# Optimization experiments

Hardware: AMD Instinct MI355X
Metric: run time of the kernel (lower is better)

## Reference

```python
import jax, jax.numpy as jnp
import numpy as np

B, H, W, C = 8, 256, 256, 180
HEADS, HEAD_DIM = 6, 30
WIN = (16, 16)
SPARSITY = 4


def setup_inputs() -> dict:
    key = jax.random.key(0)
    ks = jax.random.split(key, 6)
    bg = 1.0 / np.sqrt(3 * HEAD_DIM)          # ExpertGather init bound (1/sqrt(head_dim_out)) approx
    bs = 1.0 / np.sqrt(C * HEADS)             # ExpertScatter init bound
    return {
        "x": jax.random.normal(ks[0], (B, H, W, C), jnp.float32),
        "Wr": jax.random.normal(ks[1], (HEADS, C), jnp.float32) / np.sqrt(C),      # router Linear(dim, heads, bias=False)
        "Wqkv": jax.random.uniform(ks[2], (HEADS, C, 3 * HEAD_DIM), jnp.float32, -bg, bg),
        "Wo": jax.random.uniform(ks[3], (HEADS, HEAD_DIM, C), jnp.float32, -bs, bs),
        "Wp": jax.random.normal(ks[4], (C, C), jnp.float32) / np.sqrt(C),          # proj Linear(dim, dim)
        "bp": jnp.zeros((C,), jnp.float32),
    }


def reference(x, Wr, Wqkv, Wo, Wp, bp):
    wh, ww = WIN
    L = wh * ww  # tokens per window = 256
    # ---- window_partition: (B,H,W,C) -> (Bw, L, C)
    xw = x.reshape(B, H // wh, wh, W // ww, ww, C).transpose(0, 1, 3, 2, 4, 5).reshape(-1, L, C)
    Bw = xw.shape[0]
    # ---- router: sigmoid(Linear) -> (Bw, L, heads)
    logits = jax.nn.sigmoid(jnp.einsum('blc,ec->ble', xw, Wr))
    k = min(max(L // SPARSITY, 2), L)  # static: 64
    # ---- top-k including first token (get_topk_includefirst)
    tail = logits[:, 1:, :].transpose(0, 2, 1)          # (Bw, heads, L-1)
    tv, ti = jax.lax.top_k(tail, k - 1)                 # top k-1 over tokens 1..L-1
    ti = ti + 1
    fv = logits[:, 0, :][:, :, None]                    # (Bw, heads, 1)
    fi = jnp.zeros((Bw, HEADS, 1), jnp.int32)
    vals = jnp.concatenate([fv, tv], axis=2)            # (Bw, heads, k) sigmoid gates
    idx = jnp.concatenate([fi, ti], axis=2)             # (Bw, heads, k) token indices
    idx_flat = idx.reshape(Bw, HEADS * k)
    # ---- ExpertGather: per-head gather then per-head linear -> QKV
    Xg = jnp.take_along_axis(xw, idx_flat[:, :, None], axis=1).reshape(Bw, HEADS, k, C)
    qkv = jnp.einsum('beki,eij->bekj', Xg, Wqkv)        # (Bw, heads, k, 3*head_dim)
    Q, K, V = jnp.split(qkv, 3, axis=-1)
    # ---- scaled dot product attention over the k routed tokens per head
    scores = jnp.einsum('bekd,bejd->bekj', Q, K) / np.sqrt(HEAD_DIM).astype(np.float32)
    attn = jnp.einsum('bekj,bejd->bekd', jax.nn.softmax(scores, axis=-1), V)
    attn = attn * vals[..., None]                       # sigmoid gating
    # ---- ExpertScatter: per-head linear then scatter-add combine
    pre = jnp.einsum('bekj,eji->beki', attn, Wo)        # (Bw, heads, k, C)
    scattered = jnp.zeros((Bw, L, C), x.dtype).at[
        jnp.arange(Bw)[:, None], idx_flat
    ].add(pre.reshape(Bw, HEADS * k, C))
    # ---- window_reverse: (Bw, L, C) -> (B, H, W, C)
    y = scattered.reshape(B, H // wh, W // ww, wh, ww, C).transpose(0, 1, 3, 2, 4, 5).reshape(B, H, W, C)
    # ---- output projection (dropout prob = 0)
    return jnp.einsum('bhwc,oc->bhwo', y, Wp) + bp
```

## Files before the change

### kernel.cpp

```cpp
#include <hip/hip_runtime.h>
#include <math.h>

#define NB 8
#define NH 256
#define NW 256
#define NC 180
#define NE 6
#define HD 30
#define NL 256
#define NK 64
#define NWIN 2048

typedef __attribute__((ext_vector_type(8))) short bf16x8;
typedef __attribute__((ext_vector_type(4))) float f32x4;

union FU { bf16x8 f; unsigned u[4]; unsigned short s[8]; };

static __device__ __forceinline__ unsigned short f2bf(float x) {
    unsigned u = __float_as_uint(x);
    unsigned r = (u + 0x7FFFu + ((u >> 16) & 1u)) >> 16;
    return (unsigned short)r;
}
static __device__ __forceinline__ unsigned pk2(float a, float b) {
    return (unsigned)f2bf(a) | ((unsigned)f2bf(b) << 16);
}
static __device__ __forceinline__ bf16x8 ld8(const unsigned short* p) {
    FU t;
    *(uint2*)&t.u[0] = *(const uint2*)p;
    *(uint2*)&t.u[2] = *(const uint2*)(p + 16);
    return t.f;
}
static __device__ __forceinline__ bf16x8 ld8q(const unsigned short* p) {
    FU t;
    t.u[0] = *(const unsigned*)p;
    t.u[1] = *(const unsigned*)(p + 2);
    t.u[2] = *(const unsigned*)(p + 16);
    t.u[3] = *(const unsigned*)(p + 18);
    return t.f;
}
static __device__ __forceinline__ bf16x8 pack8(float4 a, float4 b) {
    FU t;
    t.u[0] = pk2(a.x, a.y); t.u[1] = pk2(a.z, a.w);
    t.u[2] = pk2(b.x, b.y); t.u[3] = pk2(b.z, b.w);
    return t.f;
}

__global__ __launch_bounds__(256) void k_prep(
    const float* __restrict__ Wqkv, const float* __restrict__ Wo,
    const float* __restrict__ Wp,
    unsigned short* __restrict__ Wqkv_t, unsigned short* __restrict__ Wcomb_t)
{
    int i = blockIdx.x * 256 + threadIdx.x;
    if (i < NE * 96 * 192) {
        int h = i / (96 * 192), rm = i % (96 * 192), np = rm / 192, k = rm % 192;
        int sec = np >> 5, r = np & 31;
        float v = (r < 30 && k < NC) ? Wqkv[((long)h * NC + k) * 90 + sec * 30 + r] : 0.f;
        Wqkv_t[i] = f2bf(v);
    }
    if (i < NE * 192 * 32) {
        int h = i / (192 * 32), rm = i % (192 * 32), o = rm / 32, d = rm & 31;
        float acc = 0.f;
        if (o < NC && d < HD) {
            const float* wo = Wo + ((long)h * HD + d) * NC;
            const float* wp = Wp + (long)o * NC;
            for (int c = 0; c < NC; ++c) acc += wo[c] * wp[c];
        }
        Wcomb_t[i] = f2bf(acc);
    }
}

__global__ __launch_bounds__(256) void k_router_topk(
    const float* __restrict__ x, const float* __restrict__ Wr,
    int* __restrict__ idx_g, float* __restrict__ vals_g)
{
    __shared__ float wr_s[NE * NC];
    __shared__ __align__(16) float xs[32 * 181];
    __shared__ float lg[NE * NL];

    const int w   = blockIdx.x;
    const int tid = threadIdx.x;
    const int b = w >> 8, hb = (w >> 4) & 15, wb = w & 15;
    const long win_base = (((long)b * NH + hb * 16) * NW + wb * 16) * NC;

    for (int f = tid; f < NE * NC; f += 256) wr_s[f] = Wr[f];
    __syncthreads();

    for (int tile = 0; tile < 8; ++tile) {
        for (int f = tid; f < 32 * NC; f += 256) {
            int tl = f / NC, ch = f % NC;
            int tok = tile * 32 + tl;
            int r = tok >> 4, cl = tok & 15;
            xs[tl * 181 + ch] = x[win_base + ((long)r * NW + cl) * NC + ch];
        }
        __syncthreads();
        if (tid < 192) {
            int tl = tid & 31, e = tid >> 5;
            float acc = 0.f;
            for (int c = 0; c < NC; ++c) acc += xs[tl * 181 + c] * wr_s[e * NC + c];
            lg[e * NL + tile * 32 + tl] = 1.0f / (1.0f + expf(-acc));
        }
        __syncthreads();
    }

    unsigned long long* keys = (unsigned long long*)xs;
    #pragma unroll
    for (int e = 0; e < NE; ++e) {
        unsigned kb = __float_as_uint(lg[e * NL + tid]);
        unsigned long long comp =
            ((unsigned long long)kb << 32) | (unsigned)(0xFFFFFFFFu - tid);
        if (tid == 0) comp = 0ull;
        keys[e * NL + tid] = comp;
    }
    __syncthreads();

    for (int k = 2; k <= 256; k <<= 1) {
        for (int j = k >> 1; j > 0; j >>= 1) {
            const int i = tid, ixj = i ^ j;
            if (ixj > i) {
                const bool up = ((i & k) == 0);
                #pragma unroll
                for (int e = 0; e < NE; ++e) {
                    unsigned long long a  = keys[e * NL + i];
                    unsigned long long bv = keys[e * NL + ixj];
                    bool sw = up ? (a < bv) : (a > bv);
                    if (sw) { keys[e * NL + i] = bv; keys[e * NL + ixj] = a; }
                }
            }
            __syncthreads();
        }
    }

    if (tid < NK - 1) {
        #pragma unroll
        for (int e = 0; e < NE; ++e) {
            unsigned long long kk = keys[e * NL + tid];
            int t = (int)(0xFFFFFFFFu - (unsigned)kk);
            idx_g[(w * NE + e) * NK + 1 + tid]  = t;
            vals_g[(w * NE + e) * NK + 1 + tid] = __uint_as_float((unsigned)(kk >> 32));
        }
    }
    if (tid == 0) {
        #pragma unroll
        for (int e = 0; e < NE; ++e) {
            idx_g[(w * NE + e) * NK]  = 0;
            vals_g[(w * NE + e) * NK] = lg[e * NL];
        }
    }
}

__global__ __launch_bounds__(256, 3) void k_attn(
    const float* __restrict__ x,
    const unsigned short* __restrict__ Wqkv_t,
    const int* __restrict__ idx_g, const float* __restrict__ vals_g,
    unsigned short* __restrict__ at_g)
{
    __shared__ char sm[34816];
    const int tid = threadIdx.x;
    const int wv = tid >> 6;
    const int ln = tid & 63;
    const int lr = ln & 15;
    const int lg = ln >> 4;

    const int id = blockIdx.x * 4 + wv;
    const int w = id / 6;
    const int h = id % 6;
    const int b = w >> 8, hb = (w >> 4) & 15, wb = w & 15;
    const long win_base = (((long)b * NH + hb * 16) * NW + wb * 16) * NC;

    unsigned short* q_s = (unsigned short*)(sm + wv * 8704);
    unsigned short* k_s = q_s + 2176;

    int tokr[4];
    #pragma unroll
    for (int t = 0; t < 4; ++t)
        tokr[t] = idx_g[((long)w * NE + h) * NK + 16 * t + lr];

    f32x4 acc[6][4];
    #pragma unroll
    for (int nt = 0; nt < 6; ++nt)
        #pragma unroll
        for (int mt = 0; mt < 4; ++mt) acc[nt][mt] = (f32x4){0.f, 0.f, 0.f, 0.f};

    const unsigned short* bb = Wqkv_t + ((long)h * 96 + lr) * 192 + 4 * lg;
    #pragma unroll
    for (int kt = 0; kt < 6; ++kt) {
        bf16x8 Amt[4];
        #pragma unroll
        for (int mt = 0; mt < 4; ++mt) {
            const float* xr = x + win_base +
                ((long)(tokr[mt] >> 4) * NW + (tokr[mt] & 15)) * NC;
            if (kt < 5) {
                float4 a  = *(const float4*)(xr + 4 * lg + 32 * kt);
                float4 b2 = *(const float4*)(xr + 4 * lg + 32 * kt + 16);
                Amt[mt] = pack8(a, b2);
            } else {
                float4 a  = *(const float4*)(xr + 4 * lg + 160);
                float4 b2 = make_float4(0.f, 0.f, 0.f, 0.f);
                if (lg == 0) b2 = *(const float4*)(xr + 176);
                Amt[mt] = pack8(a, b2);
            }
        }
        #pragma unroll
        for (int nt = 0; nt < 6; ++nt) {
            bf16x8 B = ld8(bb + nt * (16 * 192) + kt * 32);
            #pragma unroll
            for (int mt = 0; mt < 4; ++mt)
                acc[nt][mt] = __builtin_amdgcn_mfma_f32_16x16x32_bf16(Amt[mt], B, acc[nt][mt], 0, 0, 0);
        }
    }

    #pragma unroll
    for (int nt = 0; nt < 4; ++nt) {
        unsigned short* dst = (nt < 2 ? q_s : k_s) + 16 * (nt & 1) + lr;
        #pragma unroll
        for (int mt = 0; mt < 4; ++mt) {
            int row = 16 * mt + 4 * lg;
            dst[(row + 0) * 34] = f2bf(acc[nt][mt][0]);
            dst[(row + 1) * 34] = f2bf(acc[nt][mt][1]);
            dst[(row + 2) * 34] = f2bf(acc[nt][mt][2]);
            dst[(row + 3) * 34] = f2bf(acc[nt][mt][3]);
        }
    }
    unsigned V32[4][2][2];
    #pragma unroll
    for (int j = 0; j < 2; ++j)
        #pragma unroll
        for (int mt = 0; mt < 4; ++mt) {
            V32[mt][j][0] = pk2(acc[4 + j][mt][0], acc[4 + j][mt][1]);
            V32[mt][j][1] = pk2(acc[4 + j][mt][2], acc[4 + j][mt][3]);
        }

    __syncthreads();

    f32x4 s[4][4];
    {
        bf16x8 Bq[4];
        #pragma unroll
        for (int nt = 0; nt < 4; ++nt)
            Bq[nt] = ld8q(q_s + (16 * nt + lr) * 34 + 4 * lg);
        #pragma unroll
        for (int amt = 0; amt < 4; ++amt) {
            bf16x8 Ak = ld8q(k_s + (16 * amt + lr) * 34 + 4 * lg);
            #pragma unroll
            for (int nt = 0; nt < 4; ++nt)
                s[amt][nt] = __builtin_amdgcn_mfma_f32_16x16x32_bf16(
                    Ak, Bq[nt], (f32x4){0.f, 0.f, 0.f, 0.f}, 0, 0, 0);
        }
    }

    float gsc[4];
    #pragma unroll
    for (int nt = 0; nt < 4; ++nt) {
        float mx = -1e30f;
        #pragma unroll
        for (int amt = 0; amt < 4; ++amt)
            #pragma unroll
            for (int r = 0; r < 4; ++r) mx = fmaxf(mx, s[amt][nt][r]);
        mx = fmaxf(mx, __shfl_xor(mx, 16));
        mx = fmaxf(mx, __shfl_xor(mx, 32));
        float sum = 0.f;
        #pragma unroll
        for (int amt = 0; amt < 4; ++amt)
            #pragma unroll
            for (int r = 0; r < 4; ++r) {
                float p = __expf((s[amt][nt][r] - mx) * 0.18257418583505536f);
                s[amt][nt][r] = p;
                sum += p;
            }
        sum += __shfl_xor(sum, 16);
        sum += __shfl_xor(sum, 32);
        gsc[nt] = vals_g[((long)w * NE + h) * NK + 16 * nt + lr] / sum;
    }

    bf16x8 Av[2][2];
    #pragma unroll
    for (int amt = 0; amt < 2; ++amt)
        #pragma unroll
        for (int kt = 0; kt < 2; ++kt) {
            FU t;
            t.u[0] = V32[2 * kt][amt][0];
            t.u[1] = V32[2 * kt][amt][1];
            t.u[2] = V32[2 * kt + 1][amt][0];
            t.u[3] = V32[2 * kt + 1][amt][1];
            Av[amt][kt] = t.f;
        }
    #pragma unroll
    for (int nt = 0; nt < 4; ++nt) {
        bf16x8 Pb[2];
        float g = gsc[nt];
        #pragma unroll
        for (int kt = 0; kt < 2; ++kt) {
            FU t;
            t.u[0] = pk2(s[2 * kt][nt][0] * g, s[2 * kt][nt][1] * g);
            t.u[1] = pk2(s[2 * kt][nt][2] * g, s[2 * kt][nt][3] * g);
            t.u[2] = pk2(s[2 * kt + 1][nt][0] * g, s[2 * kt + 1][nt][1] * g);
            t.u[3] = pk2(s[2 * kt + 1][nt][2] * g, s[2 * kt + 1][nt][3] * g);
            Pb[kt] = t.f;
        }
        f32x4 a0 = (f32x4){0.f, 0.f, 0.f, 0.f};
        a0 = __builtin_amdgcn_mfma_f32_16x16x32_bf16(Av[0][0], Pb[0], a0, 0, 0, 0);
        a0 = __builtin_amdgcn_mfma_f32_16x16x32_bf16(Av[0][1], Pb[1], a0, 0, 0, 0);
        f32x4 a1 = (f32x4){0.f, 0.f, 0.f, 0.f};
        a1 = __builtin_amdgcn_mfma_f32_16x16x32_bf16(Av[1][0], Pb[0], a1, 0, 0, 0);
        a1 = __builtin_amdgcn_mfma_f32_16x16x32_bf16(Av[1][1], Pb[1], a1, 0, 0, 0);
        unsigned short* row = at_g + (((long)h * NWIN + w) * 64 + 16 * nt + lr) * 32;
        *(uint2*)(row + 4 * lg)      = make_uint2(pk2(a0[0], a0[1]), pk2(a0[2], a0[3]));
        *(uint2*)(row + 16 + 4 * lg) = make_uint2(pk2(a1[0], a1[1]), pk2(a1[2], a1[3]));
    }
}

__global__ __launch_bounds__(384, 2) void k_scatter(
    const unsigned short* __restrict__ at_g,
    const unsigned short* __restrict__ Wcomb_t,
    const float* __restrict__ bp,
    const int* __restrict__ idx_g,
    float* __restrict__ out)
{
    __shared__ float outf[256 * 49];
    __shared__ unsigned char idx_s[NE * NK];

    const int w = blockIdx.x;
    const int tid = threadIdx.x;
    const int b = w >> 8, hb = (w >> 4) & 15, wb = w & 15;

    const int wv = tid >> 6;
    const int ln = tid & 63;
    const int lr = ln & 15;
    const int lg = ln >> 4;

    idx_s[tid] = (unsigned char)idx_g[(long)w * NE * NK + tid];

    const int wcol = wv % 3;
    const int nth  = wv / 3;

    bf16x8 Bt[NE][2];
    #pragma unroll
    for (int h = 0; h < NE; ++h)
        #pragma unroll
        for (int t = 0; t < 2; ++t) {
            const int nt = 2 * nth + t;
            Bt[h][t] = ld8(at_g + (((long)h * NWIN + w) * 64 + 16 * nt + lr) * 32 + 4 * lg);
        }
    __syncthreads();

    int tokk[NE][2];
    #pragma unroll
    for (int h = 0; h < NE; ++h)
        #pragma unroll
        for (int t = 0; t < 2; ++t)
            tokk[h][t] = idx_s[h * NK + 16 * (2 * nth + t) + lr];

    #pragma unroll
    for (int p = 0; p < 4; ++p) {
        for (int f = tid; f < 256 * 49; f += 384) outf[f] = 0.f;
        __syncthreads();

        #pragma unroll
        for (int h = 0; h < NE; ++h) {
            bf16x8 Aw = ld8(Wcomb_t + ((long)h * 192 + p * 48 + 16 * wcol + lr) * 32 + 4 * lg);
            #pragma unroll
            for (int t = 0; t < 2; ++t) {
                f32x4 acc = __builtin_amdgcn_mfma_f32_16x16x32_bf16(
                    Aw, Bt[h][t], (f32x4){0.f, 0.f, 0.f, 0.f}, 0, 0, 0);
                float* dst = outf + tokk[h][t] * 49 + 16 * wcol + 4 * lg;
                dst[0] += acc[0];
                dst[1] += acc[1];
                dst[2] += acc[2];
                dst[3] += acc[3];
            }
            __syncthreads();
        }

        const int nf4 = (p == 3) ? 9 : 12;
        for (int f = tid; f < 256 * nf4; f += 384) {
            int t = f / nf4, j = f % nf4;
            int c = 48 * p + 4 * j;
            float4 o;
            o.x = outf[t * 49 + 4 * j]     + bp[c];
            o.y = outf[t * 49 + 4 * j + 1] + bp[c + 1];
            o.z = outf[t * 49 + 4 * j + 2] + bp[c + 2];
            o.w = outf[t * 49 + 4 * j + 3] + bp[c + 3];
            long obase = (((long)b * NH + hb * 16 + (t >> 4)) * NW + wb * 16 + (t & 15)) * NC + c;
            *(float4*)(out + obase) = o;
        }
        __syncthreads();
    }
}

extern "C" void kernel_launch(void* const* d_in, const int* in_sizes, int n_in,
                              void* d_out, int out_size, void* d_ws, size_t ws_size,
                              hipStream_t stream) {
    const float* x    = (const float*)d_in[0];
    const float* Wr   = (const float*)d_in[1];
    const float* Wqkv = (const float*)d_in[2];
    const float* Wo   = (const float*)d_in[3];
    const float* Wp   = (const float*)d_in[4];
    const float* bp   = (const float*)d_in[5];
    float* out = (float*)d_out;

    char* ws = (char*)d_ws;
    unsigned short* Wqkv_t  = (unsigned short*)ws;
    unsigned short* Wcomb_t = (unsigned short*)(ws + 221184);
    int*   idx_g  = (int*)(ws + 294912);
    float* vals_g = (float*)(ws + 294912 + (size_t)NWIN * NE * NK * 4);
    unsigned short* at_g = (unsigned short*)(ws + 294912 + 2 * (size_t)NWIN * NE * NK * 4);

    k_prep<<<432, 256, 0, stream>>>(Wqkv, Wo, Wp, Wqkv_t, Wcomb_t);
    k_router_topk<<<NWIN, 256, 0, stream>>>(x, Wr, idx_g, vals_g);
    k_attn<<<3072, 256, 0, stream>>>(x, Wqkv_t, idx_g, vals_g, at_g);
    k_scatter<<<NWIN, 384, 0, stream>>>(at_g, Wcomb_t, bp, idx_g, out);
}
```

Before: 598.5 us.

## Pre-swizzle bf16 weight and attention layouts for 16-byte vector loads; remap block order

Reorders the packed Wqkv, combined Wo·Wp and attention-output buffers so that each lane's eight MFMA operand elements are contiguous. Two 8-byte loads become one 16-byte load in the attention and scatter kernels, and the attention store becomes a single 16-byte write. It also permutes the attention kernel's block index, likely to spread work across XCDs or improve cache locality. The layout has to stay consistent between the producer and consumer kernels, and the gains are limited to operand-load instruction count.

Result: faster. 569.4 us (-4.9%).

```diff
diff --git a/kernel.cpp b/kernel.cpp
--- a/kernel.cpp
+++ b/kernel.cpp
@@ -30,6 +30,11 @@
     *(uint2*)&t.u[2] = *(const uint2*)(p + 16);
     return t.f;
 }
+static __device__ __forceinline__ bf16x8 ld16(const unsigned short* p) {
+    FU t;
+    *(uint4*)&t.u[0] = *(const uint4*)p;
+    return t.f;
+}
 static __device__ __forceinline__ bf16x8 ld8q(const unsigned short* p) {
     FU t;
     t.u[0] = *(const unsigned*)p;
@@ -52,13 +57,19 @@
 {
     int i = blockIdx.x * 256 + threadIdx.x;
     if (i < NE * 96 * 192) {
-        int h = i / (96 * 192), rm = i % (96 * 192), np = rm / 192, k = rm % 192;
+        int q = i / 192, rem = i % 192;
+        int h = q / 96, np = q % 96;
+        int kt = rem / 32, lg = (rem % 32) / 8, e = rem % 8;
+        int k = 32 * kt + 4 * lg + (e < 4 ? e : 12 + e);
         int sec = np >> 5, r = np & 31;
         float v = (r < 30 && k < NC) ? Wqkv[((long)h * NC + k) * 90 + sec * 30 + r] : 0.f;
         Wqkv_t[i] = f2bf(v);
     }
     if (i < NE * 192 * 32) {
-        int h = i / (192 * 32), rm = i % (192 * 32), o = rm / 32, d = rm & 31;
+        int q = i / 32, rem = i % 32;
+        int h = q / 192, o = q % 192;
+        int lg = rem / 8, e = rem % 8;
+        int d = 4 * lg + (e < 4 ? e : 12 + e);
         float acc = 0.f;
         if (o < NC && d < HD) {
             const float* wo = Wo + ((long)h * HD + d) * NC;
@@ -161,7 +172,8 @@
     const int lr = ln & 15;
     const int lg = ln >> 4;
 
-    const int id = blockIdx.x * 4 + wv;
+    const int bid = (blockIdx.x & 7) * 384 + (blockIdx.x >> 3);
+    const int id = bid * 4 + wv;
     const int w = id / 6;
     const int h = id % 6;
     const int b = w >> 8, hb = (w >> 4) & 15, wb = w & 15;
@@ -181,7 +193,7 @@
         #pragma unroll
         for (int mt = 0; mt < 4; ++mt) acc[nt][mt] = (f32x4){0.f, 0.f, 0.f, 0.f};
 
-    const unsigned short* bb = Wqkv_t + ((long)h * 96 + lr) * 192 + 4 * lg;
+    const unsigned short* bb = Wqkv_t + ((long)h * 96 + lr) * 192 + 8 * lg;
     #pragma unroll
     for (int kt = 0; kt < 6; ++kt) {
         bf16x8 Amt[4];
@@ -202,7 +214,7 @@
         }
         #pragma unroll
         for (int nt = 0; nt < 6; ++nt) {
-            bf16x8 B = ld8(bb + nt * (16 * 192) + kt * 32);
+            bf16x8 B = ld16(bb + nt * (16 * 192) + kt * 32);
             #pragma unroll
             for (int mt = 0; mt < 4; ++mt)
                 acc[nt][mt] = __builtin_amdgcn_mfma_f32_16x16x32_bf16(Amt[mt], B, acc[nt][mt], 0, 0, 0);
@@ -303,9 +315,9 @@
         f32x4 a1 = (f32x4){0.f, 0.f, 0.f, 0.f};
         a1 = __builtin_amdgcn_mfma_f32_16x16x32_bf16(Av[1][0], Pb[0], a1, 0, 0, 0);
         a1 = __builtin_amdgcn_mfma_f32_16x16x32_bf16(Av[1][1], Pb[1], a1, 0, 0, 0);
-        unsigned short* row = at_g + (((long)h * NWIN + w) * 64 + 16 * nt + lr) * 32;
-        *(uint2*)(row + 4 * lg)      = make_uint2(pk2(a0[0], a0[1]), pk2(a0[2], a0[3]));
-        *(uint2*)(row + 16 + 4 * lg) = make_uint2(pk2(a1[0], a1[1]), pk2(a1[2], a1[3]));
+        unsigned short* row = at_g + (((long)h * NWIN + w) * 64 + 16 * nt + lr) * 32 + 8 * lg;
+        *(uint4*)row = make_uint4(pk2(a0[0], a0[1]), pk2(a0[2], a0[3]),
+                                  pk2(a1[0], a1[1]), pk2(a1[2], a1[3]));
     }
 }
 
@@ -339,7 +351,7 @@
         #pragma unroll
         for (int t = 0; t < 2; ++t) {
             const int nt = 2 * nth + t;
-            Bt[h][t] = ld8(at_g + (((long)h * NWIN + w) * 64 + 16 * nt + lr) * 32 + 4 * lg);
+            Bt[h][t] = ld16(at_g + (((long)h * NWIN + w) * 64 + 16 * nt + lr) * 32 + 8 * lg);
         }
     __syncthreads();
 
@@ -357,7 +369,7 @@
 
         #pragma unroll
         for (int h = 0; h < NE; ++h) {
-            bf16x8 Aw = ld8(Wcomb_t + ((long)h * 192 + p * 48 + 16 * wcol + lr) * 32 + 4 * lg);
+            bf16x8 Aw = ld16(Wcomb_t + ((long)h * 192 + p * 48 + 16 * wcol + lr) * 32 + 8 * lg);
             #pragma unroll
             for (int t = 0; t < 2; ++t) {
                 f32x4 acc = __builtin_amdgcn_mfma_f32_16x16x32_bf16(
```
